# Kernel optimization log

Hardware: AMD Instinct MI355X
Metric: run time of the kernel (lower is better)

Reference implementation:

```python
import jax, jax.numpy as jnp
import numpy as np

NTOK, HIDDEN, FFN, NEXP, TOPK = 8192, 2048, 2048, 8, 2
M = NTOK * TOPK          # total scattered rows
CAP = M // NEXP          # equal per-expert split (fixed for jit)


def setup_inputs() -> dict:
    key = jax.random.key(0)
    k1, k2, k3 = jax.random.split(key, 3)
    inputs_shard = jax.random.normal(k1, (NTOK, HIDDEN), dtype=jnp.float32)
    # flux grouped-GEMM weight layout: [experts, out_features, in_features]
    w1 = jax.random.normal(k2, (NEXP, FFN, HIDDEN), dtype=jnp.float32) * (HIDDEN ** -0.5)
    w2 = jax.random.normal(k3, (NEXP, HIDDEN, FFN), dtype=jnp.float32) * (FFN ** -0.5)
    # scatter_index[t, k] = destination row in the expert-sorted buffer.
    # arange is a valid permutation of [0, M): contiguous CAP-sized blocks per expert.
    scatter_index = jnp.arange(M, dtype=jnp.int32).reshape(NTOK, TOPK)
    return {"inputs_shard": inputs_shard, "w1": w1, "w2": w2,
            "scatter_index": scatter_index}


def reference(inputs_shard, w1, w2, scatter_index):
    # --- AG-scatter dispatch: replicate each token topk times and scatter
    # into the expert-sorted buffer (rows grouped by expert, CAP per expert).
    x_rep = jnp.repeat(inputs_shard, TOPK, axis=0)                  # [M, H]
    x_scat = jnp.zeros((M, HIDDEN), inputs_shard.dtype)
    x_scat = x_scat.at[scatter_index.reshape(-1)].set(x_rep)        # [M, H]

    # --- grouped GEMM fc1 (equal splits -> batched einsum over experts)
    xg = x_scat.reshape(NEXP, CAP, HIDDEN)                          # [E, CAP, H]
    h = jnp.einsum('ech,efh->ecf', xg, w1)                          # [E, CAP, F]
    h = jax.nn.gelu(h, approximate=False)

    # --- grouped GEMM fc2
    y = jnp.einsum('ecf,ehf->ech', h, w2).reshape(M, HIDDEN)        # [M, H]

    # --- gather-RS combine: sum the topk expert outputs per token
    out = y[scatter_index].sum(axis=1)                              # [NTOK, H]
    return out
```

## Files before the change

kernel.cpp:

```cpp
#include <hip/hip_runtime.h>
#include <hip/hip_bf16.h>
#include <math.h>

#define NTOK   8192
#define HIDDEN 2048
#define FFN_   2048
#define NEXP   8
#define TOPK   2
#define MTOT   (NTOK*TOPK)
#define CAP    (MTOT/NEXP)
#define KD     2048
#define NT     32

typedef __bf16 bf16_t;
typedef __attribute__((ext_vector_type(8))) __bf16 bf16x8;
typedef __attribute__((ext_vector_type(4))) __bf16 bf16x4;
typedef __attribute__((ext_vector_type(4))) float  f32x4;

__device__ __forceinline__ void async16(const bf16_t* g, bf16_t* l) {
    __builtin_amdgcn_global_load_lds(
        (const __attribute__((address_space(1))) void*)g,
        (__attribute__((address_space(3))) void*)l, 16, 0, 0);
}

#define FENCE() asm volatile("" ::: "memory")
#define BAR()   do { FENCE(); __builtin_amdgcn_s_barrier(); FENCE(); } while (0)

__global__ void k_prep(const int* __restrict__ scat, int* __restrict__ inv,
                       int* __restrict__ flag) {
    int i = blockIdx.x * 256 + threadIdx.x;
    inv[scat[i]] = i;
    if (i < NTOK && ((scat[2 * i] ^ scat[2 * i + 1]) != 1)) atomicOr(flag, 1);
}

__device__ __forceinline__ void cast4(const float* __restrict__ s,
                                      bf16_t* __restrict__ d, size_t i) {
    float4 v = ((const float4*)s)[i];
    bf16x4 o;
    o[0] = (bf16_t)v.x; o[1] = (bf16_t)v.y; o[2] = (bf16_t)v.z; o[3] = (bf16_t)v.w;
    ((bf16x4*)d)[i] = o;
}

__global__ __launch_bounds__(256)
void k_cast_all(const float* __restrict__ x,  const float* __restrict__ w1,
                const float* __restrict__ w2, bf16_t* __restrict__ xb,
                bf16_t* __restrict__ w1b, bf16_t* __restrict__ w2b) {
    const size_t QX = (size_t)NTOK * HIDDEN / 4;
    const size_t QW = (size_t)NEXP * FFN_ * HIDDEN / 4;
    size_t t0     = (size_t)blockIdx.x * 256 + threadIdx.x;
    size_t stride = (size_t)gridDim.x * 256;
    for (size_t i = t0; i < QX; i += stride) cast4(x,  xb,  i);
    for (size_t i = t0; i < QW; i += stride) cast4(w1, w1b, i);
    for (size_t i = t0; i < QW; i += stride) cast4(w2, w2b, i);
}

template <int EPI>
__global__ __launch_bounds__(512, 2)
void k_gemm(const bf16_t* __restrict__ A, const bf16_t* __restrict__ B,
            bf16_t* __restrict__ Hout, float* __restrict__ Out,
            const int* __restrict__ inv, const int* __restrict__ flag)
{
    const int paired = (*flag == 0);
    const int per_e  = paired ? 32 : 64;
    int idx = blockIdx.x >> 3;
    int e   = blockIdx.x & 7;
    if (idx >= per_e) return;
    int row0 = (idx >> 3) * 256;
    int col0 = (idx & 7) * 256;
    const int Mcap = paired ? 1024 : 2048;
    const bf16_t* Be = B + (size_t)e * 2048 * KD;

    __shared__ __align__(16) bf16_t lds[2 * 2 * 16384];

    int tid  = threadIdx.x;
    int lane = tid & 63;
    int wid  = tid >> 6;
    int wm   = wid >> 2;
    int wn   = wid & 3;

    int rr = tid >> 3;
    int g8 = ((tid & 7) ^ (rr & 7)) * 8;
    const bf16_t* ap[2][2];
    const bf16_t* bp[2][2];
    #pragma unroll
    for (int h = 0; h < 2; h++)
        #pragma unroll
        for (int l = 0; l < 2; l++) {
            int ra = row0 + h * 128 + l * 64 + rr;
            if (EPI == 0) {
                int sidx = paired ? 2 * (e * 1024 + ra) : (e * 2048 + ra);
                ap[h][l] = A + (size_t)(inv[sidx] / TOPK) * KD + g8;
            } else {
                ap[h][l] = A + ((size_t)e * Mcap + ra) * KD + g8;
            }
            bp[h][l] = Be + (size_t)(col0 + h * 128 + l * 64 + rr) * KD + g8;
        }

#define STG(m_, pp, h_, jt) do { \
        bf16_t* d_ = lds + (((jt) & 1) * 32768 + (m_) * 16384 + (h_) * 8192 + tid * 8); \
        async16(pp[h_][0] + (size_t)(jt) * 64, d_); \
        async16(pp[h_][1] + (size_t)(jt) * 64, d_ + 4096); \
    } while (0)

    int lm  = lane & 15;
    int lkq = lane >> 4;
    int sw  = (lane & 7) << 4;
    int cA0 = ((lkq * 16) ^ sw) >> 1;
    int cA1 = ((64 + lkq * 16) ^ sw) >> 1;

    f32x4  acc[8][4] = {};
    bf16x8 af[4][2];
    bf16x8 bfn[2][2];
    bf16x8 bf1[2][2];

#define LOADA(qm) do { _Pragma("unroll") \
        for (int i = 0; i < 4; i++) { \
            const bf16_t* rp_ = Ab + (wm * 128 + (qm) * 64 + i * 16 + lm) * 64; \
            af[i][0] = *(const bf16x8*)(rp_ + cA0); \
            af[i][1] = *(const bf16x8*)(rp_ + cA1); } } while (0)

#define LOADB1() do { _Pragma("unroll") \
        for (int jj = 0; jj < 2; jj++) { \
            const bf16_t* rp_ = Bb + (wn * 64 + 32 + jj * 16 + lm) * 64; \
            bf1[jj][0] = *(const bf16x8*)(rp_ + cA0); \
            bf1[jj][1] = *(const bf16x8*)(rp_ + cA1); } } while (0)

#define LOADB0N(Bsrc) do { _Pragma("unroll") \
        for (int jj = 0; jj < 2; jj++) { \
            const bf16_t* rp_ = (Bsrc) + (wn * 64 + jj * 16 + lm) * 64; \
            bfn[jj][0] = *(const bf16x8*)(rp_ + cA0); \
            bfn[jj][1] = *(const bf16x8*)(rp_ + cA1); } } while (0)

#define MFMAQ(qm, BARR) do { \
        __builtin_amdgcn_s_setprio(1); \
        _Pragma("unroll") \
        for (int i = 0; i < 4; i++) \
            _Pragma("unroll") \
            for (int jj = 0; jj < 2; jj++) { \
                acc[(qm)*4+i][(BQ)*2+jj] = __builtin_amdgcn_mfma_f32_16x16x32_bf16( \
                    af[i][0], BARR[jj][0], acc[(qm)*4+i][(BQ)*2+jj], 0, 0, 0); \
                acc[(qm)*4+i][(BQ)*2+jj] = __builtin_amdgcn_mfma_f32_16x16x32_bf16( \
                    af[i][1], BARR[jj][1], acc[(qm)*4+i][(BQ)*2+jj], 0, 0, 0); \
            } \
        __builtin_amdgcn_s_setprio(0); \
    } while (0)

    STG(0, ap, 0, 0); STG(0, ap, 1, 0); STG(1, bp, 0, 0); STG(1, bp, 1, 0);
    STG(0, ap, 0, 1); STG(1, bp, 0, 1); STG(1, bp, 1, 1);
    asm volatile("s_waitcnt vmcnt(6)" ::: "memory");
    BAR();
    {
        const bf16_t* Bb0 = lds + 16384;
        LOADB0N(Bb0);
    }

    for (int j = 0; j < NT; ++j) {
        const bf16_t* Ab = lds + (j & 1) * 32768;
        const bf16_t* Bb = Ab + 16384;
        LOADA(0);
        if (j + 1 < NT) STG(0, ap, 1, j + 1);
        BAR();
        { enum { BQ = 0 }; MFMAQ(0, bfn); }
        BAR();
        LOADB1();
        BAR();
        { enum { BQ = 1 }; MFMAQ(0, bf1); }
        BAR();
        LOADA(1);
        if (j + 2 < NT) { STG(1, bp, 0, j + 2); STG(1, bp, 1, j + 2); }
        BAR();
        { enum { BQ = 0 }; MFMAQ(1, bfn); }
        BAR();
        if (j + 2 < NT) {
            STG(0, ap, 0, j + 2);
            asm volatile("s_waitcnt vmcnt(6)" ::: "memory");
        } else if (j + 1 < NT) {
            asm volatile("s_waitcnt vmcnt(0)" ::: "memory");
        }
        BAR();
        if (j + 1 < NT) {
            const bf16_t* Bbn = lds + (((j + 1) & 1) * 32768) + 16384;
            LOADB0N(Bbn);
        }
        { enum { BQ = 1 }; MFMAQ(1, bf1); }
        BAR();
    }

    int rbase = lkq * 4;
    if (EPI == 0) {
        #pragma unroll
        for (int mi = 0; mi < 8; mi++) {
            int row = row0 + wm * 128 + mi * 16 + rbase;
            #pragma unroll
            for (int nj = 0; nj < 4; nj++) {
                int col = col0 + wn * 64 + nj * 16 + lm;
                #pragma unroll
                for (int r = 0; r < 4; r++) {
                    float v = acc[mi][nj][r];
                    v = 0.5f * v * (1.0f + erff(v * 0.70710678118f));
                    Hout[((size_t)e * Mcap + row + r) * FFN_ + col] = (bf16_t)v;
                }
            }
        }
    } else if (paired) {
        #pragma unroll
        for (int mi = 0; mi < 8; mi++) {
            #pragma unroll
            for (int r = 0; r < 4; r++) {
                int u   = e * 1024 + row0 + wm * 128 + mi * 16 + rbase + r;
                int tok = inv[2 * u] / TOPK;
                #pragma unroll
                for (int nj = 0; nj < 4; nj++) {
                    int col = col0 + wn * 64 + nj * 16 + lm;
                    Out[(size_t)tok * HIDDEN + col] = 2.0f * acc[mi][nj][r];
                }
            }
        }
    } else {
        #pragma unroll
        for (int mi = 0; mi < 8; mi++) {
            #pragma unroll
            for (int r = 0; r < 4; r++) {
                int gm  = e * 2048 + row0 + wm * 128 + mi * 16 + rbase + r;
                int tok = inv[gm] / TOPK;
                #pragma unroll
                for (int nj = 0; nj < 4; nj++) {
                    int col = col0 + wn * 64 + nj * 16 + lm;
                    atomicAdd(&Out[(size_t)tok * HIDDEN + col], acc[mi][nj][r]);
                }
            }
        }
    }
#undef STG
#undef LOADA
#undef LOADB1
#undef LOADB0N
#undef MFMAQ
}

extern "C" void kernel_launch(void* const* d_in, const int* in_sizes, int n_in,
                              void* d_out, int out_size, void* d_ws, size_t ws_size,
                              hipStream_t stream) {
    const float* x    = (const float*)d_in[0];
    const float* w1   = (const float*)d_in[1];
    const float* w2   = (const float*)d_in[2];
    const int*   scat = (const int*)d_in[3];
    float* out = (float*)d_out;

    char* ws = (char*)d_ws;
    size_t off = 0;
    int*    inv   = (int*)(ws + off);   off += 65536;
    int*    flagp = (int*)(ws + off);   off += 256;
    bf16_t* xbt = (bf16_t*)(ws + off);  off += (size_t)NTOK * HIDDEN * 2;
    bf16_t* w1b = (bf16_t*)(ws + off);  off += (size_t)NEXP * FFN_ * HIDDEN * 2;
    bf16_t* w2b = (bf16_t*)(ws + off);  off += (size_t)NEXP * HIDDEN * FFN_ * 2;
    bf16_t* hb  = (bf16_t*)(ws + off);  off += (size_t)MTOT * FFN_ * 2;

    hipMemsetAsync(d_out, 0, (size_t)out_size * sizeof(float), stream);
    hipMemsetAsync(flagp, 0, 4, stream);

    k_prep<<<MTOT / 256, 256, 0, stream>>>(scat, inv, flagp);
    k_cast_all<<<2048, 256, 0, stream>>>(x, w1, w2, xbt, w1b, w2b);

    k_gemm<0><<<NEXP * 64, 512, 0, stream>>>(xbt, w1b, hb, nullptr, inv, flagp);
    k_gemm<1><<<NEXP * 64, 512, 0, stream>>>(hb, w2b, nullptr, out, inv, flagp);
}
```

Measured before the change: 500.3 us.

## Load fp32 weights directly in GEMM and convert to bf16 in LDS staging

Removes the separate weight cast pass: each GEMM now reads fp32 weights through registers, converts them to bf16 and writes them swizzled into LDS, pipelined two k-steps ahead. The x cast is folded into the prep kernel. The output memset becomes a conditional zero kernel that skips when tokens are paired, since the paired epilogue writes directly. This saves a full read-write pass over both weight tensors, at the cost of reading twice the weight bytes per tile inside the GEMM, more register pressure, and giving up async global-to-LDS copies for B.

```diff
diff --git a/kernel.cpp b/kernel.cpp
--- a/kernel.cpp
+++ b/kernel.cpp
@@ -14,7 +14,6 @@
 
 typedef __bf16 bf16_t;
 typedef __attribute__((ext_vector_type(8))) __bf16 bf16x8;
-typedef __attribute__((ext_vector_type(4))) __bf16 bf16x4;
 typedef __attribute__((ext_vector_type(4))) float  f32x4;
 
 __device__ __forceinline__ void async16(const bf16_t* g, bf16_t* l) {
@@ -26,37 +25,39 @@
 #define FENCE() asm volatile("" ::: "memory")
 #define BAR()   do { FENCE(); __builtin_amdgcn_s_barrier(); FENCE(); } while (0)
 
-__global__ void k_prep(const int* __restrict__ scat, int* __restrict__ inv,
-                       int* __restrict__ flag) {
-    int i = blockIdx.x * 256 + threadIdx.x;
-    inv[scat[i]] = i;
-    if (i < NTOK && ((scat[2 * i] ^ scat[2 * i + 1]) != 1)) atomicOr(flag, 1);
-}
-
-__device__ __forceinline__ void cast4(const float* __restrict__ s,
-                                      bf16_t* __restrict__ d, size_t i) {
-    float4 v = ((const float4*)s)[i];
-    bf16x4 o;
-    o[0] = (bf16_t)v.x; o[1] = (bf16_t)v.y; o[2] = (bf16_t)v.z; o[3] = (bf16_t)v.w;
-    ((bf16x4*)d)[i] = o;
-}
-
 __global__ __launch_bounds__(256)
-void k_cast_all(const float* __restrict__ x,  const float* __restrict__ w1,
-                const float* __restrict__ w2, bf16_t* __restrict__ xb,
-                bf16_t* __restrict__ w1b, bf16_t* __restrict__ w2b) {
+void k_prep(const int* __restrict__ scat, int* __restrict__ inv,
+            int* __restrict__ flag, const float* __restrict__ x,
+            bf16_t* __restrict__ xb) {
+    int b = blockIdx.x, t = threadIdx.x;
+    if (b < MTOT / 256) {
+        int i = b * 256 + t;
+        inv[scat[i]] = i;
+        if (i < NTOK && ((scat[2 * i] ^ scat[2 * i + 1]) != 1)) atomicOr(flag, 1);
+    }
     const size_t QX = (size_t)NTOK * HIDDEN / 4;
-    const size_t QW = (size_t)NEXP * FFN_ * HIDDEN / 4;
-    size_t t0     = (size_t)blockIdx.x * 256 + threadIdx.x;
+    size_t t0 = (size_t)b * 256 + t, stride = (size_t)gridDim.x * 256;
+    for (size_t i = t0; i < QX; i += stride) {
+        float4 v = ((const float4*)x)[i];
+        __attribute__((ext_vector_type(4))) __bf16 o;
+        o[0] = (bf16_t)v.x; o[1] = (bf16_t)v.y; o[2] = (bf16_t)v.z; o[3] = (bf16_t)v.w;
+        ((__attribute__((ext_vector_type(4))) __bf16*)xb)[i] = o;
+    }
+}
+
+__global__ __launch_bounds__(256)
+void k_zero(float* __restrict__ out, const int* __restrict__ flag) {
+    if (*flag == 0) return;
+    const size_t QO = (size_t)NTOK * HIDDEN / 4;
+    size_t t0 = (size_t)blockIdx.x * 256 + threadIdx.x;
     size_t stride = (size_t)gridDim.x * 256;
-    for (size_t i = t0; i < QX; i += stride) cast4(x,  xb,  i);
-    for (size_t i = t0; i < QW; i += stride) cast4(w1, w1b, i);
-    for (size_t i = t0; i < QW; i += stride) cast4(w2, w2b, i);
+    float4 z = {0.f, 0.f, 0.f, 0.f};
+    for (size_t i = t0; i < QO; i += stride) ((float4*)out)[i] = z;
 }
 
 template <int EPI>
 __global__ __launch_bounds__(512, 2)
-void k_gemm(const bf16_t* __restrict__ A, const bf16_t* __restrict__ B,
+void k_gemm(const bf16_t* __restrict__ A, const float* __restrict__ B,
             bf16_t* __restrict__ Hout, float* __restrict__ Out,
             const int* __restrict__ inv, const int* __restrict__ flag)
 {
@@ -68,7 +69,7 @@
     int row0 = (idx >> 3) * 256;
     int col0 = (idx & 7) * 256;
     const int Mcap = paired ? 1024 : 2048;
-    const bf16_t* Be = B + (size_t)e * 2048 * KD;
+    const float* Bf = B + (size_t)e * 2048 * KD;
 
     __shared__ __align__(16) bf16_t lds[2 * 2 * 16384];
 
@@ -81,7 +82,6 @@
     int rr = tid >> 3;
     int g8 = ((tid & 7) ^ (rr & 7)) * 8;
     const bf16_t* ap[2][2];
-    const bf16_t* bp[2][2];
     #pragma unroll
     for (int h = 0; h < 2; h++)
         #pragma unroll
@@ -93,14 +93,35 @@
             } else {
                 ap[h][l] = A + ((size_t)e * Mcap + ra) * KD + g8;
             }
-            bp[h][l] = Be + (size_t)(col0 + h * 128 + l * 64 + rr) * KD + g8;
-        }
-
-#define STG(m_, pp, h_, jt) do { \
-        bf16_t* d_ = lds + (((jt) & 1) * 32768 + (m_) * 16384 + (h_) * 8192 + tid * 8); \
-        async16(pp[h_][0] + (size_t)(jt) * 64, d_); \
-        async16(pp[h_][1] + (size_t)(jt) * 64, d_ + 4096); \
+        }
+
+    int rr2 = tid >> 1;
+    int kh  = (tid & 1) * 32;
+    const float* bqf = Bf + ((size_t)(col0 + rr2)) * KD + kh;
+    float4 bld[4];
+
+#define STGA(h_, jt) do { \
+        bf16_t* d_ = lds + (((jt) & 1) * 32768 + (h_) * 8192 + tid * 8); \
+        async16(ap[h_][0] + (size_t)(jt) * 64, d_); \
+        async16(ap[h_][1] + (size_t)(jt) * 64, d_ + 4096); \
     } while (0)
+
+#define BLDH(jt, half) do { _Pragma("unroll") \
+        for (int q = 0; q < 4; q++) \
+            bld[q] = ((const float4*)(bqf + (size_t)(jt) * 64))[(half) * 4 + q]; \
+    } while (0)
+
+#define BWRH(jt, half) do { \
+        char* bb_ = (char*)(lds + ((jt) & 1) * 32768 + 16384); \
+        _Pragma("unroll") \
+        for (int q = 0; q < 2; q++) { \
+            float4 u_ = bld[2 * q], v_ = bld[2 * q + 1]; \
+            bf16x8 o_; \
+            o_[0]=(bf16_t)u_.x; o_[1]=(bf16_t)u_.y; o_[2]=(bf16_t)u_.z; o_[3]=(bf16_t)u_.w; \
+            o_[4]=(bf16_t)v_.x; o_[5]=(bf16_t)v_.y; o_[6]=(bf16_t)v_.z; o_[7]=(bf16_t)v_.w; \
+            int kk_ = kh + (half) * 16 + q * 8; \
+            *(bf16x8*)(bb_ + ((rr2 * 128 + kk_ * 2) ^ ((rr2 & 7) << 4))) = o_; \
+        } } while (0)
 
     int lm  = lane & 15;
     int lkq = lane >> 4;
@@ -145,9 +166,10 @@
         __builtin_amdgcn_s_setprio(0); \
     } while (0)
 
-    STG(0, ap, 0, 0); STG(0, ap, 1, 0); STG(1, bp, 0, 0); STG(1, bp, 1, 0);
-    STG(0, ap, 0, 1); STG(1, bp, 0, 1); STG(1, bp, 1, 1);
-    asm volatile("s_waitcnt vmcnt(6)" ::: "memory");
+    STGA(0, 0); STGA(1, 0); STGA(0, 1);
+    BLDH(0, 0); BWRH(0, 0); BLDH(0, 1); BWRH(0, 1);
+    BLDH(1, 0); BWRH(1, 0); BLDH(1, 1); BWRH(1, 1);
+    asm volatile("s_waitcnt vmcnt(2) lgkmcnt(0)" ::: "memory");
     BAR();
     {
         const bf16_t* Bb0 = lds + 16384;
@@ -158,7 +180,8 @@
         const bf16_t* Ab = lds + (j & 1) * 32768;
         const bf16_t* Bb = Ab + 16384;
         LOADA(0);
-        if (j + 1 < NT) STG(0, ap, 1, j + 1);
+        if (j + 2 < NT) BLDH(j + 2, 0);
+        if (j + 1 < NT) STGA(1, j + 1);
         BAR();
         { enum { BQ = 0 }; MFMAQ(0, bfn); }
         BAR();
@@ -167,13 +190,14 @@
         { enum { BQ = 1 }; MFMAQ(0, bf1); }
         BAR();
         LOADA(1);
-        if (j + 2 < NT) { STG(1, bp, 0, j + 2); STG(1, bp, 1, j + 2); }
+        if (j + 2 < NT) { BWRH(j + 2, 0); BLDH(j + 2, 1); }
         BAR();
         { enum { BQ = 0 }; MFMAQ(1, bfn); }
         BAR();
         if (j + 2 < NT) {
-            STG(0, ap, 0, j + 2);
-            asm volatile("s_waitcnt vmcnt(6)" ::: "memory");
+            BWRH(j + 2, 1);
+            STGA(0, j + 2);
+            asm volatile("s_waitcnt vmcnt(2) lgkmcnt(0)" ::: "memory");
         } else if (j + 1 < NT) {
             asm volatile("s_waitcnt vmcnt(0)" ::: "memory");
         }
@@ -231,7 +255,9 @@
             }
         }
     }
-#undef STG
+#undef STGA
+#undef BLDH
+#undef BWRH
 #undef LOADA
 #undef LOADB1
 #undef LOADB0N
@@ -252,16 +278,13 @@
     int*    inv   = (int*)(ws + off);   off += 65536;
     int*    flagp = (int*)(ws + off);   off += 256;
     bf16_t* xbt = (bf16_t*)(ws + off);  off += (size_t)NTOK * HIDDEN * 2;
-    bf16_t* w1b = (bf16_t*)(ws + off);  off += (size_t)NEXP * FFN_ * HIDDEN * 2;
-    bf16_t* w2b = (bf16_t*)(ws + off);  off += (size_t)NEXP * HIDDEN * FFN_ * 2;
     bf16_t* hb  = (bf16_t*)(ws + off);  off += (size_t)MTOT * FFN_ * 2;
 
-    hipMemsetAsync(d_out, 0, (size_t)out_size * sizeof(float), stream);
     hipMemsetAsync(flagp, 0, 4, stream);
 
-    k_prep<<<MTOT / 256, 256, 0, stream>>>(scat, inv, flagp);
-    k_cast_all<<<2048, 256, 0, stream>>>(x, w1, w2, xbt, w1b, w2b);
-
-    k_gemm<0><<<NEXP * 64, 512, 0, stream>>>(xbt, w1b, hb, nullptr, inv, flagp);
-    k_gemm<1><<<NEXP * 64, 512, 0, stream>>>(hb, w2b, nullptr, out, inv, flagp);
-}
+    k_prep<<<2048, 256, 0, stream>>>(scat, inv, flagp, x, xbt);
+    k_zero<<<2048, 256, 0, stream>>>(out, flagp);
+
+    k_gemm<0><<<NEXP * 64, 512, 0, stream>>>(xbt, w1, hb, nullptr, inv, flagp);
+    k_gemm<1><<<NEXP * 64, 512, 0, stream>>>(hb, w2, nullptr, out, inv, flagp);
+}
```

Result: slower. 566.7 us (+13.3%).
